# Kernel tuning notes

Measured on AMD Instinct MI355X. Metric: run time of the kernel, lower is better.

## Reference

```python
import jax, jax.numpy as jnp
import numpy as np

NUM_USERS = 100000
NUM_ITEMS = 50000
EMB = 64
E_U = 1200000
E_I = 600000


def setup_inputs() -> dict:
    key = jax.random.key(0)
    k1, k2, k3, k4 = jax.random.split(key, 4)
    return {
        "user_edge_index": jax.random.randint(k1, (2, E_U), 0, NUM_USERS, dtype=jnp.int32),
        "item_edge_index": jax.random.randint(k2, (2, E_I), 0, NUM_ITEMS, dtype=jnp.int32),
        "W_user": jax.random.normal(k3, (NUM_USERS, EMB), dtype=jnp.float32) * 0.1,
        "b_user": jnp.zeros((EMB,), dtype=jnp.float32),
        "W_item": jax.random.normal(k4, (NUM_ITEMS, EMB), dtype=jnp.float32) * 0.1,
        "b_item": jnp.zeros((EMB,), dtype=jnp.float32),
    }


def _gcn(W, b, edge_index, n):
    # x = I, so x @ kernel == kernel (W).  GCN renorm: relu(D^-1/2 (A+I) D^-1/2 W + b)
    self_loops = jnp.arange(n, dtype=edge_index.dtype)
    row = jnp.concatenate([edge_index[0], self_loops])
    col = jnp.concatenate([edge_index[1], self_loops])
    deg = jax.ops.segment_sum(jnp.ones(row.shape[0], dtype=W.dtype), row, num_segments=n)
    inv_sqrt = jnp.where(deg > 0, jax.lax.rsqrt(jnp.maximum(deg, 1e-12)), 0.0)
    norm = inv_sqrt[row] * inv_sqrt[col]           # [E+n]
    msgs = W[col] * norm[:, None]                  # gather + scale: [E+n, EMB]
    agg = jax.ops.segment_sum(msgs, row, num_segments=n)  # scatter-add: [n, EMB]
    return jax.nn.relu(agg + b)


def reference(user_edge_index, item_edge_index, W_user, b_user, W_item, b_item):
    user_h = _gcn(W_user, b_user, user_edge_index, NUM_USERS)
    item_h = _gcn(W_item, b_item, item_edge_index, NUM_ITEMS)
    return (user_h, item_h)
```

## Files before the change

kernel.cpp:

```cpp
#include <hip/hip_runtime.h>
#include <hip/hip_fp16.h>

#define NUSERS 100000
#define NITEMS 50000
#define EMB 64
#define BROWS 256
#define CHUNK 4096
#define MAXB 512
#define CAP  4096
#define NTOH 1024
#define NB_U ((NUSERS + BROWS - 1) / BROWS)
#define NB_I ((NITEMS + BROWS - 1) / BROWS)


__global__ void build1_kernel(const int* __restrict__ rowU, const int* __restrict__ rowI,
                              unsigned* __restrict__ bcntU, unsigned* __restrict__ bcntI,
                              unsigned* __restrict__ pairsU, unsigned* __restrict__ pairsI,
                              const float* __restrict__ WU, const float* __restrict__ WI,
                              __half* __restrict__ WhU, __half* __restrict__ WhI,
                              int EU, int EI, int gbU, int gbTot) {
    __shared__ unsigned h[MAXB];
    __shared__ unsigned base[MAXB];
    int t = threadIdx.x;
    if ((int)blockIdx.x >= gbTot) {
        int nt = (int)gridDim.x - gbTot;
        const int T4U = NUSERS * (EMB / 4), T4I = NITEMS * (EMB / 4);
        for (int i = ((int)blockIdx.x - gbTot) * 256 + t; i < T4U + T4I; i += nt * 256) {
            const float4* W; __half2* Wh2; int idx;
            if (i < T4U) { W = (const float4*)WU; Wh2 = (__half2*)WhU; idx = i; }
            else         { W = (const float4*)WI; Wh2 = (__half2*)WhI; idx = i - T4U; }
            float4 w = W[idx];
            Wh2[2 * idx]     = __floats2half2_rn(w.x, w.y);
            Wh2[2 * idx + 1] = __floats2half2_rn(w.z, w.w);
        }
        return;
    }
    const int* row; const int* col; unsigned* bcnt; unsigned* pairs; int E, blk;
    if ((int)blockIdx.x < gbU) { row = rowU; col = rowU + EU; bcnt = bcntU; pairs = pairsU; E = EU; blk = blockIdx.x; }
    else                       { row = rowI; col = rowI + EI; bcnt = bcntI; pairs = pairsI; E = EI; blk = blockIdx.x - gbU; }
    for (int i = t; i < MAXB; i += 256) h[i] = 0;
    __syncthreads();
    int lo = blk * CHUNK, hi = min(lo + CHUNK, E);
    int m = hi - lo;
    int m4 = m >> 2;
    const int4* r4 = (const int4*)(row + lo);
    int4 rr[4];
    int  ng = 0;
    #pragma unroll
    for (int j = 0; j < 4; j++) {
        int i = t + j * 256;
        if (i < m4) {
            rr[j] = r4[i];
            ng = j + 1;
            atomicAdd(&h[rr[j].x >> 8], 1u);
            atomicAdd(&h[rr[j].y >> 8], 1u);
            atomicAdd(&h[rr[j].z >> 8], 1u);
            atomicAdd(&h[rr[j].w >> 8], 1u);
        }
    }
    int rtail = 0;
    if (t < (m & 3)) {
        rtail = row[lo + (m4 << 2) + t];
        atomicAdd(&h[rtail >> 8], 1u);
    }
    __syncthreads();
    for (int i = t; i < MAXB; i += 256) {
        unsigned cnt = h[i];
        base[i] = cnt ? ((unsigned)i * CAP + atomicAdd(&bcnt[i], cnt)) : 0u;
        h[i] = 0;
    }
    __syncthreads();
    const int4* c4 = (const int4*)(col + lo);
    #pragma unroll
    for (int j = 0; j < 4; j++) {
        if (j < ng) {
            int i = t + j * 256;
            int4 r = rr[j];
            int4 c = c4[i];
            int b0 = r.x >> 8, b1 = r.y >> 8, b2 = r.z >> 8, b3 = r.w >> 8;
            unsigned p0 = base[b0] + atomicAdd(&h[b0], 1u);
            unsigned p1 = base[b1] + atomicAdd(&h[b1], 1u);
            unsigned p2 = base[b2] + atomicAdd(&h[b2], 1u);
            unsigned p3 = base[b3] + atomicAdd(&h[b3], 1u);
            pairs[p0] = ((unsigned)(r.x & 255) << 20) | (unsigned)c.x;
            pairs[p1] = ((unsigned)(r.y & 255) << 20) | (unsigned)c.y;
            pairs[p2] = ((unsigned)(r.z & 255) << 20) | (unsigned)c.z;
            pairs[p3] = ((unsigned)(r.w & 255) << 20) | (unsigned)c.w;
        }
    }
    if (t < (m & 3)) {
        int c = col[lo + (m4 << 2) + t];
        int b0 = rtail >> 8;
        unsigned p = base[b0] + atomicAdd(&h[b0], 1u);
        pairs[p] = ((unsigned)(rtail & 255) << 20) | (unsigned)c;
    }
}

__global__ void bprep_kernel(const unsigned* __restrict__ bcntU, const unsigned* __restrict__ bcntI,
                             const unsigned* __restrict__ pairsU, const unsigned* __restrict__ pairsI,
                             uint2* __restrict__ odU, uint2* __restrict__ odI,
                             float* __restrict__ invU, float* __restrict__ invI,
                             int* __restrict__ colsU, int* __restrict__ colsI,
                             unsigned* __restrict__ totU, unsigned* __restrict__ totI) {
    __shared__ unsigned d[BROWS];
    __shared__ unsigned cur[BROWS];
    __shared__ unsigned stage[CAP];
    __shared__ unsigned wsum[4];
    __shared__ unsigned sbase;
    const unsigned* bcnt; const unsigned* pairs; uint2* od; float* inv; int* cols; unsigned* tot; int n, b;
    if ((int)blockIdx.x < NB_U) { bcnt = bcntU; pairs = pairsU; od = odU; inv = invU; cols = colsU; tot = totU; n = NUSERS; b = blockIdx.x; }
    else                        { bcnt = bcntI; pairs = pairsI; od = odI; inv = invI; cols = colsI; tot = totI; n = NITEMS; b = blockIdx.x - NB_U; }
    int t = threadIdx.x;
    int lane = t & 63, wid = t >> 6;
    int rbase = b * BROWS;
    d[t] = 0;
    __syncthreads();
    unsigned cnt = min(bcnt[b], (unsigned)CAP);
    unsigned lo = (unsigned)b * CAP;
    unsigned cnt4 = cnt >> 2;
    const uint4* p4 = (const uint4*)(pairs + lo);
    for (unsigned i = t; i < cnt4; i += 256) {
        uint4 pk = p4[i];
        ((uint4*)stage)[i] = pk;
        atomicAdd(&d[pk.x >> 20], 1u);
        atomicAdd(&d[pk.y >> 20], 1u);
        atomicAdd(&d[pk.z >> 20], 1u);
        atomicAdd(&d[pk.w >> 20], 1u);
    }
    if (t < (int)(cnt & 3u)) {
        unsigned pk = pairs[lo + (cnt4 << 2) + t];
        stage[(cnt4 << 2) + t] = pk;
        atomicAdd(&d[pk >> 20], 1u);
    }
    __syncthreads();
    unsigned v0 = d[t];
    unsigned x = v0;
    #pragma unroll
    for (int off = 1; off < 64; off <<= 1) {
        unsigned y = __shfl_up(x, off, 64);
        if (lane >= off) x += y;
    }
    if (lane == 63) wsum[wid] = x;
    __syncthreads();
    unsigned wbase = 0;
    #pragma unroll
    for (int wj = 0; wj < 4; wj++) wbase += (wj < wid) ? wsum[wj] : 0u;
    if (t == 0) sbase = atomicAdd(tot, wsum[0] + wsum[1] + wsum[2] + wsum[3]);
    __syncthreads();
    unsigned running = sbase + wbase + x - v0;
    int idx = rbase + t;
    if (idx < n) {
        od[idx] = make_uint2(running, v0);
        inv[idx] = rsqrtf((float)(v0 + 1u));
        cur[t] = running;
    }
    __syncthreads();
    for (unsigned i = t; i < cnt4; i += 256) {
        uint4 pk = ((const uint4*)stage)[i];
        unsigned p0 = atomicAdd(&cur[pk.x >> 20], 1u);
        unsigned p1 = atomicAdd(&cur[pk.y >> 20], 1u);
        unsigned p2 = atomicAdd(&cur[pk.z >> 20], 1u);
        unsigned p3 = atomicAdd(&cur[pk.w >> 20], 1u);
        cols[p0] = (int)(pk.x & 0xFFFFFu);
        cols[p1] = (int)(pk.y & 0xFFFFFu);
        cols[p2] = (int)(pk.z & 0xFFFFFu);
        cols[p3] = (int)(pk.w & 0xFFFFFu);
    }
    if (t < (int)(cnt & 3u)) {
        unsigned pk = stage[(cnt4 << 2) + t];
        unsigned p = atomicAdd(&cur[pk >> 20], 1u);
        cols[p] = (int)(pk & 0xFFFFFu);
    }
}

__global__ void tohalf_kernel(const float* __restrict__ WU, const float* __restrict__ WI,
                              __half* __restrict__ WhU, __half* __restrict__ WhI) {
    const int T4U = NUSERS * (EMB / 4), T4I = NITEMS * (EMB / 4);
    for (int i = blockIdx.x * 256 + threadIdx.x; i < T4U + T4I; i += gridDim.x * 256) {
        const float4* W; __half2* Wh2; int idx;
        if (i < T4U) { W = (const float4*)WU; Wh2 = (__half2*)WhU; idx = i; }
        else         { W = (const float4*)WI; Wh2 = (__half2*)WhI; idx = i - T4U; }
        float4 w = W[idx];
        Wh2[2 * idx]     = __floats2half2_rn(w.x, w.y);
        Wh2[2 * idx + 1] = __floats2half2_rn(w.z, w.w);
    }
}

__device__ __forceinline__ void accs(float* acc, float4 f, float ic) {
    const __half2* h = (const __half2*)&f;
    #pragma unroll
    for (int j = 0; j < 4; j++) {
        float2 tv = __half22float2(h[j]);
        acc[2 * j]     += tv.x * ic;
        acc[2 * j + 1] += tv.y * ic;
    }
}

__global__ void gather2h_kernel(const uint2* __restrict__ odU, const uint2* __restrict__ odI,
                                const int* __restrict__ colsU, const int* __restrict__ colsI,
                                const __half* __restrict__ WhU, const __half* __restrict__ WhI,
                                const float* __restrict__ bU, const float* __restrict__ bI,
                                const float* __restrict__ invU, const float* __restrict__ invI,
                                float* __restrict__ outU, float* __restrict__ outI, int ggU) {
    const uint2* od; const int* cols; const __half* Wh; const float* bb; const float* inv;
    float* out; int n, r0;
    if ((int)blockIdx.x < ggU) { od = odU; cols = colsU; Wh = WhU; bb = bU; inv = invU; out = outU; n = NUSERS; r0 = blockIdx.x * 32; }
    else                       { od = odI; cols = colsI; Wh = WhI; bb = bI; inv = invI; out = outI; n = NITEMS; r0 = (blockIdx.x - ggU) * 32; }
    int r = r0 + (threadIdx.x >> 3);
    if (r >= n) return;
    int d8 = threadIdx.x & 7;
    uint2 o = od[r];
    unsigned k = o.x, end = o.x + o.y;
    const __half* wb = Wh + d8 * 8;
    float acc[8] = {0.f, 0.f, 0.f, 0.f, 0.f, 0.f, 0.f, 0.f};
    for (; k + 4 <= end; k += 4) {
        int c0 = cols[k];
        int c1 = cols[k + 1];
        int c2 = cols[k + 2];
        int c3 = cols[k + 3];
        float i0 = inv[c0], i1 = inv[c1], i2 = inv[c2], i3 = inv[c3];
        float4 f0 = *(const float4*)(wb + (size_t)c0 * EMB);
        float4 f1 = *(const float4*)(wb + (size_t)c1 * EMB);
        float4 f2 = *(const float4*)(wb + (size_t)c2 * EMB);
        float4 f3 = *(const float4*)(wb + (size_t)c3 * EMB);
        accs(acc, f0, i0); accs(acc, f1, i1); accs(acc, f2, i2); accs(acc, f3, i3);
    }
    for (; k < end; ++k) {
        int c0 = cols[k];
        float i0 = inv[c0];
        float4 f0 = *(const float4*)(wb + (size_t)c0 * EMB);
        accs(acc, f0, i0);
    }
    float inv_r = inv[r];
    float4 fs = *(const float4*)(Wh + (size_t)r * EMB + d8 * 8);
    accs(acc, fs, inv_r);
    const float4 bv0 = *(const float4*)(bb + d8 * 8);
    const float4 bv1 = *(const float4*)(bb + d8 * 8 + 4);
    float4 o0, o1;
    o0.x = fmaxf(acc[0] * inv_r + bv0.x, 0.f);
    o0.y = fmaxf(acc[1] * inv_r + bv0.y, 0.f);
    o0.z = fmaxf(acc[2] * inv_r + bv0.z, 0.f);
    o0.w = fmaxf(acc[3] * inv_r + bv0.w, 0.f);
    o1.x = fmaxf(acc[4] * inv_r + bv1.x, 0.f);
    o1.y = fmaxf(acc[5] * inv_r + bv1.y, 0.f);
    o1.z = fmaxf(acc[6] * inv_r + bv1.z, 0.f);
    o1.w = fmaxf(acc[7] * inv_r + bv1.w, 0.f);
    *(float4*)(out + (size_t)r * EMB + d8 * 8)     = o0;
    *(float4*)(out + (size_t)r * EMB + d8 * 8 + 4) = o1;
}

__global__ void gather2f_kernel(const uint2* __restrict__ odU, const uint2* __restrict__ odI,
                                const int* __restrict__ colsU, const int* __restrict__ colsI,
                                const float* __restrict__ WU, const float* __restrict__ WI,
                                const float* __restrict__ bU, const float* __restrict__ bI,
                                const float* __restrict__ invU, const float* __restrict__ invI,
                                float* __restrict__ outU, float* __restrict__ outI, int ggU) {
    const uint2* od; const int* cols; const float* W; const float* bb; const float* inv;
    float* out; int n, r0;
    if ((int)blockIdx.x < ggU) { od = odU; cols = colsU; W = WU; bb = bU; inv = invU; out = outU; n = NUSERS; r0 = blockIdx.x * 32; }
    else                       { od = odI; cols = colsI; W = WI; bb = bI; inv = invI; out = outI; n = NITEMS; r0 = (blockIdx.x - ggU) * 32; }
    int r = r0 + (threadIdx.x >> 3);
    if (r >= n) return;
    int d8 = threadIdx.x & 7;
    uint2 o = od[r];
    unsigned k = o.x, end = o.x + o.y;
    const float* wb = W + d8 * 8;
    float acc[8] = {0.f, 0.f, 0.f, 0.f, 0.f, 0.f, 0.f, 0.f};
    for (; k < end; ++k) {
        int c0 = cols[k];
        float ic = inv[c0];
        float4 f0 = *(const float4*)(wb + (size_t)c0 * EMB);
        float4 f1 = *(const float4*)(wb + (size_t)c0 * EMB + 4);
        acc[0] += f0.x * ic; acc[1] += f0.y * ic; acc[2] += f0.z * ic; acc[3] += f0.w * ic;
        acc[4] += f1.x * ic; acc[5] += f1.y * ic; acc[6] += f1.z * ic; acc[7] += f1.w * ic;
    }
    float inv_r = inv[r];
    float4 s0 = *(const float4*)(W + (size_t)r * EMB + d8 * 8);
    float4 s1 = *(const float4*)(W + (size_t)r * EMB + d8 * 8 + 4);
    const float4 bv0 = *(const float4*)(bb + d8 * 8);
    const float4 bv1 = *(const float4*)(bb + d8 * 8 + 4);
    float4 o0, o1;
    o0.x = fmaxf((acc[0] + s0.x * inv_r) * inv_r + bv0.x, 0.f);
    o0.y = fmaxf((acc[1] + s0.y * inv_r) * inv_r + bv0.y, 0.f);
    o0.z = fmaxf((acc[2] + s0.z * inv_r) * inv_r + bv0.z, 0.f);
    o0.w = fmaxf((acc[3] + s0.w * inv_r) * inv_r + bv0.w, 0.f);
    o1.x = fmaxf((acc[4] + s1.x * inv_r) * inv_r + bv1.x, 0.f);
    o1.y = fmaxf((acc[5] + s1.y * inv_r) * inv_r + bv1.y, 0.f);
    o1.z = fmaxf((acc[6] + s1.z * inv_r) * inv_r + bv1.z, 0.f);
    o1.w = fmaxf((acc[7] + s1.w * inv_r) * inv_r + bv1.w, 0.f);
    *(float4*)(out + (size_t)r * EMB + d8 * 8)     = o0;
    *(float4*)(out + (size_t)r * EMB + d8 * 8 + 4) = o1;
}

extern "C" void kernel_launch(void* const* d_in, const int* in_sizes, int n_in,
                              void* d_out, int out_size, void* d_ws, size_t ws_size,
                              hipStream_t stream) {
    const int*   ue = (const int*)d_in[0];
    const int*   ie = (const int*)d_in[1];
    const float* Wu = (const float*)d_in[2];
    const float* bu = (const float*)d_in[3];
    const float* Wi = (const float*)d_in[4];
    const float* bi = (const float*)d_in[5];

    const int E_U = in_sizes[0] / 2;
    const int E_I = in_sizes[1] / 2;

    float* out_u = (float*)d_out;
    float* out_i = out_u + (size_t)NUSERS * EMB;

    unsigned* w       = (unsigned*)d_ws;
    unsigned* bcnt_u  = w;            w += MAXB;
    unsigned* bcnt_i  = w;            w += MAXB;
    unsigned* tot_u   = w;            w += 1;
    unsigned* tot_i   = w;            w += 1;
    uint2*    od_u    = (uint2*)w;    w += 2 * (size_t)NUSERS;
    uint2*    od_i    = (uint2*)w;    w += 2 * (size_t)NITEMS;
    float*    inv_u   = (float*)w;    w += NUSERS;
    float*    inv_i   = (float*)w;    w += NITEMS;
    int*      cols_u  = (int*)w;      w += E_U;
    int*      cols_i  = (int*)w;      w += E_I;
    w += (size_t)(-(intptr_t)(w - (unsigned*)d_ws)) & 3;

    const size_t pairs_words = (size_t)(NB_U + NB_I) * CAP;
    const size_t wh_words    = (size_t)(NUSERS + NITEMS) * EMB / 2;
    unsigned* pairs_u = w;
    unsigned* pairs_i = w + (size_t)NB_U * CAP;
    const size_t need_A = (size_t)((char*)(w + pairs_words + wh_words) - (char*)d_ws);
    const size_t need_B = (size_t)((char*)(w + (pairs_words > wh_words ? pairs_words : wh_words)) - (char*)d_ws);
    const bool pathA = (ws_size >= need_A);
    const bool pathB = (!pathA && ws_size >= need_B);
    __half* wh_u = pathA ? (__half*)(w + pairs_words) : (__half*)w;
    __half* wh_i = wh_u + (size_t)NUSERS * EMB;

    hipMemsetAsync(bcnt_u, 0, (2 * MAXB + 2) * sizeof(unsigned), stream);

    const int gb_u  = (E_U + CHUNK - 1) / CHUNK;
    const int gb_i  = (E_I + CHUNK - 1) / CHUNK;
    const int gbTot = gb_u + gb_i;
    const int gg_u  = (NUSERS + 31) / 32;
    const int gg_i  = (NITEMS + 31) / 32;

    if (pathA) {
        build1_kernel <<<gbTot + NTOH, 256, 0, stream>>>(ue, ie, bcnt_u, bcnt_i, pairs_u, pairs_i,
                                                         Wu, Wi, wh_u, wh_i, E_U, E_I, gb_u, gbTot);
        bprep_kernel  <<<NB_U + NB_I, 256, 0, stream>>>(bcnt_u, bcnt_i, pairs_u, pairs_i,
                                                        od_u, od_i, inv_u, inv_i,
                                                        cols_u, cols_i, tot_u, tot_i);
        gather2h_kernel<<<gg_u + gg_i, 256, 0, stream>>>(od_u, od_i, cols_u, cols_i,
                                                         wh_u, wh_i, bu, bi, inv_u, inv_i,
                                                         out_u, out_i, gg_u);
    } else if (pathB) {
        build1_kernel <<<gbTot, 256, 0, stream>>>(ue, ie, bcnt_u, bcnt_i, pairs_u, pairs_i,
                                                  Wu, Wi, wh_u, wh_i, E_U, E_I, gb_u, gbTot);
        bprep_kernel  <<<NB_U + NB_I, 256, 0, stream>>>(bcnt_u, bcnt_i, pairs_u, pairs_i,
                                                        od_u, od_i, inv_u, inv_i,
                                                        cols_u, cols_i, tot_u, tot_i);
        tohalf_kernel <<<2048, 256, 0, stream>>>(Wu, Wi, wh_u, wh_i);
        gather2h_kernel<<<gg_u + gg_i, 256, 0, stream>>>(od_u, od_i, cols_u, cols_i,
                                                         wh_u, wh_i, bu, bi, inv_u, inv_i,
                                                         out_u, out_i, gg_u);
    } else {
        build1_kernel <<<gbTot, 256, 0, stream>>>(ue, ie, bcnt_u, bcnt_i, pairs_u, pairs_i,
                                                  Wu, Wi, (__half*)nullptr, (__half*)nullptr,
                                                  E_U, E_I, gb_u, gbTot);
        bprep_kernel  <<<NB_U + NB_I, 256, 0, stream>>>(bcnt_u, bcnt_i, pairs_u, pairs_i,
                                                        od_u, od_i, inv_u, inv_i,
                                                        cols_u, cols_i, tot_u, tot_i);
        gather2f_kernel<<<gg_u + gg_i, 256, 0, stream>>>(od_u, od_i, cols_u, cols_i,
                                                         Wu, Wi, bu, bi, inv_u, inv_i,
                                                         out_u, out_i, gg_u);
    }
}
```

Baseline: 111.9 us.

## Pre-scale half-precision weights by inverse sqrt degree during bucket prep

Moves the fp32-to-fp16 weight conversion out of the edge-bucketing kernel and into the per-row prep kernel, where each row is multiplied by its inverse sqrt degree before conversion. The gather kernel then sums the pre-scaled half rows directly and no longer loads a random inv[col] value per edge. This removes one dependent random load and a multiply per edge. In exchange the conversion now runs after degrees are known, so it can no longer overlap with bucketing, and rounding the scaled values to fp16 changes precision slightly.

```diff
diff --git a/kernel.cpp b/kernel.cpp
--- a/kernel.cpp
+++ b/kernel.cpp
@@ -8,7 +8,6 @@
 #define CHUNK 4096
 #define MAXB 512
 #define CAP  4096
-#define NTOH 1024
 #define NB_U ((NUSERS + BROWS - 1) / BROWS)
 #define NB_I ((NITEMS + BROWS - 1) / BROWS)
 
@@ -16,25 +15,10 @@
 __global__ void build1_kernel(const int* __restrict__ rowU, const int* __restrict__ rowI,
                               unsigned* __restrict__ bcntU, unsigned* __restrict__ bcntI,
                               unsigned* __restrict__ pairsU, unsigned* __restrict__ pairsI,
-                              const float* __restrict__ WU, const float* __restrict__ WI,
-                              __half* __restrict__ WhU, __half* __restrict__ WhI,
-                              int EU, int EI, int gbU, int gbTot) {
+                              int EU, int EI, int gbU) {
     __shared__ unsigned h[MAXB];
     __shared__ unsigned base[MAXB];
     int t = threadIdx.x;
-    if ((int)blockIdx.x >= gbTot) {
-        int nt = (int)gridDim.x - gbTot;
-        const int T4U = NUSERS * (EMB / 4), T4I = NITEMS * (EMB / 4);
-        for (int i = ((int)blockIdx.x - gbTot) * 256 + t; i < T4U + T4I; i += nt * 256) {
-            const float4* W; __half2* Wh2; int idx;
-            if (i < T4U) { W = (const float4*)WU; Wh2 = (__half2*)WhU; idx = i; }
-            else         { W = (const float4*)WI; Wh2 = (__half2*)WhI; idx = i - T4U; }
-            float4 w = W[idx];
-            Wh2[2 * idx]     = __floats2half2_rn(w.x, w.y);
-            Wh2[2 * idx + 1] = __floats2half2_rn(w.z, w.w);
-        }
-        return;
-    }
     const int* row; const int* col; unsigned* bcnt; unsigned* pairs; int E, blk;
     if ((int)blockIdx.x < gbU) { row = rowU; col = rowU + EU; bcnt = bcntU; pairs = pairsU; E = EU; blk = blockIdx.x; }
     else                       { row = rowI; col = rowI + EI; bcnt = bcntI; pairs = pairsI; E = EI; blk = blockIdx.x - gbU; }
@@ -101,18 +85,24 @@
                              uint2* __restrict__ odU, uint2* __restrict__ odI,
                              float* __restrict__ invU, float* __restrict__ invI,
                              int* __restrict__ colsU, int* __restrict__ colsI,
-                             unsigned* __restrict__ totU, unsigned* __restrict__ totI) {
+                             unsigned* __restrict__ totU, unsigned* __restrict__ totI,
+                             const float* __restrict__ WU, const float* __restrict__ WI,
+                             __half* __restrict__ WhU, __half* __restrict__ WhI,
+                             int doConv) {
     __shared__ unsigned d[BROWS];
     __shared__ unsigned cur[BROWS];
+    __shared__ float    invl[BROWS];
     __shared__ unsigned stage[CAP];
     __shared__ unsigned wsum[4];
     __shared__ unsigned sbase;
-    const unsigned* bcnt; const unsigned* pairs; uint2* od; float* inv; int* cols; unsigned* tot; int n, b;
-    if ((int)blockIdx.x < NB_U) { bcnt = bcntU; pairs = pairsU; od = odU; inv = invU; cols = colsU; tot = totU; n = NUSERS; b = blockIdx.x; }
-    else                        { bcnt = bcntI; pairs = pairsI; od = odI; inv = invI; cols = colsI; tot = totI; n = NITEMS; b = blockIdx.x - NB_U; }
+    const unsigned* bcnt; const unsigned* pairs; uint2* od; float* inv; int* cols;
+    unsigned* tot; const float* W; __half* Wh; int n, b;
+    if ((int)blockIdx.x < NB_U) { bcnt = bcntU; pairs = pairsU; od = odU; inv = invU; cols = colsU; tot = totU; W = WU; Wh = WhU; n = NUSERS; b = blockIdx.x; }
+    else                        { bcnt = bcntI; pairs = pairsI; od = odI; inv = invI; cols = colsI; tot = totI; W = WI; Wh = WhI; n = NITEMS; b = blockIdx.x - NB_U; }
     int t = threadIdx.x;
     int lane = t & 63, wid = t >> 6;
     int rbase = b * BROWS;
+    int nrows = min(BROWS, n - rbase);
     d[t] = 0;
     __syncthreads();
     unsigned cnt = min(bcnt[b], (unsigned)CAP);
@@ -148,11 +138,13 @@
     if (t == 0) sbase = atomicAdd(tot, wsum[0] + wsum[1] + wsum[2] + wsum[3]);
     __syncthreads();
     unsigned running = sbase + wbase + x - v0;
+    float iv = rsqrtf((float)(v0 + 1u));
     int idx = rbase + t;
     if (idx < n) {
         od[idx] = make_uint2(running, v0);
-        inv[idx] = rsqrtf((float)(v0 + 1u));
+        inv[idx] = iv;
         cur[t] = running;
+        invl[t] = iv;
     }
     __syncthreads();
     for (unsigned i = t; i < cnt4; i += 256) {
@@ -171,28 +163,40 @@
         unsigned p = atomicAdd(&cur[pk >> 20], 1u);
         cols[p] = (int)(pk & 0xFFFFFu);
     }
+    if (doConv) {
+        const float4* W4 = (const float4*)W + (size_t)rbase * 16;
+        __half2* Wh2 = (__half2*)Wh + (size_t)rbase * 32;
+        for (int i = t; i < nrows * 16; i += 256) {
+            float s = invl[i >> 4];
+            float4 wv = W4[i];
+            Wh2[2 * i]     = __floats2half2_rn(wv.x * s, wv.y * s);
+            Wh2[2 * i + 1] = __floats2half2_rn(wv.z * s, wv.w * s);
+        }
+    }
 }
 
 __global__ void tohalf_kernel(const float* __restrict__ WU, const float* __restrict__ WI,
+                              const float* __restrict__ invU, const float* __restrict__ invI,
                               __half* __restrict__ WhU, __half* __restrict__ WhI) {
     const int T4U = NUSERS * (EMB / 4), T4I = NITEMS * (EMB / 4);
     for (int i = blockIdx.x * 256 + threadIdx.x; i < T4U + T4I; i += gridDim.x * 256) {
-        const float4* W; __half2* Wh2; int idx;
-        if (i < T4U) { W = (const float4*)WU; Wh2 = (__half2*)WhU; idx = i; }
-        else         { W = (const float4*)WI; Wh2 = (__half2*)WhI; idx = i - T4U; }
+        const float4* W; const float* inv; __half2* Wh2; int idx;
+        if (i < T4U) { W = (const float4*)WU; inv = invU; Wh2 = (__half2*)WhU; idx = i; }
+        else         { W = (const float4*)WI; inv = invI; Wh2 = (__half2*)WhI; idx = i - T4U; }
+        float s = inv[idx >> 4];
         float4 w = W[idx];
-        Wh2[2 * idx]     = __floats2half2_rn(w.x, w.y);
-        Wh2[2 * idx + 1] = __floats2half2_rn(w.z, w.w);
-    }
-}
-
-__device__ __forceinline__ void accs(float* acc, float4 f, float ic) {
+        Wh2[2 * idx]     = __floats2half2_rn(w.x * s, w.y * s);
+        Wh2[2 * idx + 1] = __floats2half2_rn(w.z * s, w.w * s);
+    }
+}
+
+__device__ __forceinline__ void acc8(float* acc, float4 f) {
     const __half2* h = (const __half2*)&f;
     #pragma unroll
     for (int j = 0; j < 4; j++) {
         float2 tv = __half22float2(h[j]);
-        acc[2 * j]     += tv.x * ic;
-        acc[2 * j + 1] += tv.y * ic;
+        acc[2 * j]     += tv.x;
+        acc[2 * j + 1] += tv.y;
     }
 }
 
@@ -218,22 +222,20 @@
         int c1 = cols[k + 1];
         int c2 = cols[k + 2];
         int c3 = cols[k + 3];
-        float i0 = inv[c0], i1 = inv[c1], i2 = inv[c2], i3 = inv[c3];
         float4 f0 = *(const float4*)(wb + (size_t)c0 * EMB);
         float4 f1 = *(const float4*)(wb + (size_t)c1 * EMB);
         float4 f2 = *(const float4*)(wb + (size_t)c2 * EMB);
         float4 f3 = *(const float4*)(wb + (size_t)c3 * EMB);
-        accs(acc, f0, i0); accs(acc, f1, i1); accs(acc, f2, i2); accs(acc, f3, i3);
+        acc8(acc, f0); acc8(acc, f1); acc8(acc, f2); acc8(acc, f3);
     }
     for (; k < end; ++k) {
         int c0 = cols[k];
-        float i0 = inv[c0];
         float4 f0 = *(const float4*)(wb + (size_t)c0 * EMB);
-        accs(acc, f0, i0);
+        acc8(acc, f0);
     }
     float inv_r = inv[r];
     float4 fs = *(const float4*)(Wh + (size_t)r * EMB + d8 * 8);
-    accs(acc, fs, inv_r);
+    acc8(acc, fs);
     const float4 bv0 = *(const float4*)(bb + d8 * 8);
     const float4 bv1 = *(const float4*)(bb + d8 * 8 + 4);
     float4 o0, o1;
@@ -340,32 +342,30 @@
     const int gg_u  = (NUSERS + 31) / 32;
     const int gg_i  = (NITEMS + 31) / 32;
 
+    build1_kernel<<<gbTot, 256, 0, stream>>>(ue, ie, bcnt_u, bcnt_i, pairs_u, pairs_i,
+                                             E_U, E_I, gb_u);
     if (pathA) {
-        build1_kernel <<<gbTot + NTOH, 256, 0, stream>>>(ue, ie, bcnt_u, bcnt_i, pairs_u, pairs_i,
-                                                         Wu, Wi, wh_u, wh_i, E_U, E_I, gb_u, gbTot);
         bprep_kernel  <<<NB_U + NB_I, 256, 0, stream>>>(bcnt_u, bcnt_i, pairs_u, pairs_i,
                                                         od_u, od_i, inv_u, inv_i,
-                                                        cols_u, cols_i, tot_u, tot_i);
+                                                        cols_u, cols_i, tot_u, tot_i,
+                                                        Wu, Wi, wh_u, wh_i, 1);
         gather2h_kernel<<<gg_u + gg_i, 256, 0, stream>>>(od_u, od_i, cols_u, cols_i,
                                                          wh_u, wh_i, bu, bi, inv_u, inv_i,
                                                          out_u, out_i, gg_u);
     } else if (pathB) {
-        build1_kernel <<<gbTot, 256, 0, stream>>>(ue, ie, bcnt_u, bcnt_i, pairs_u, pairs_i,
-                                                  Wu, Wi, wh_u, wh_i, E_U, E_I, gb_u, gbTot);
         bprep_kernel  <<<NB_U + NB_I, 256, 0, stream>>>(bcnt_u, bcnt_i, pairs_u, pairs_i,
                                                         od_u, od_i, inv_u, inv_i,
-                                                        cols_u, cols_i, tot_u, tot_i);
-        tohalf_kernel <<<2048, 256, 0, stream>>>(Wu, Wi, wh_u, wh_i);
+                                                        cols_u, cols_i, tot_u, tot_i,
+                                                        Wu, Wi, wh_u, wh_i, 0);
+        tohalf_kernel <<<2048, 256, 0, stream>>>(Wu, Wi, inv_u, inv_i, wh_u, wh_i);
         gather2h_kernel<<<gg_u + gg_i, 256, 0, stream>>>(od_u, od_i, cols_u, cols_i,
                                                          wh_u, wh_i, bu, bi, inv_u, inv_i,
                                                          out_u, out_i, gg_u);
     } else {
-        build1_kernel <<<gbTot, 256, 0, stream>>>(ue, ie, bcnt_u, bcnt_i, pairs_u, pairs_i,
-                                                  Wu, Wi, (__half*)nullptr, (__half*)nullptr,
-                                                  E_U, E_I, gb_u, gbTot);
         bprep_kernel  <<<NB_U + NB_I, 256, 0, stream>>>(bcnt_u, bcnt_i, pairs_u, pairs_i,
                                                         od_u, od_i, inv_u, inv_i,
-                                                        cols_u, cols_i, tot_u, tot_i);
+                                                        cols_u, cols_i, tot_u, tot_i,
+                                                        Wu, Wi, (__half*)nullptr, (__half*)nullptr, 0);
         gather2f_kernel<<<gg_u + gg_i, 256, 0, stream>>>(od_u, od_i, cols_u, cols_i,
                                                          Wu, Wi, bu, bi, inv_u, inv_i,
                                                          out_u, out_i, gg_u);
```

After: 111.3 us. About the same (-0.5%).
